# Performance work log

Hardware: AMD Instinct MI355X
Metric: run time of the kernel (lower is better)

Reference implementation:

```python
import jax, jax.numpy as jnp
import numpy as np

STRIDE = 16
A = 9
PRE_NMS_TOP_N = 6000
POST_NMS_TOP_N = 300
NMS_THRESH = 0.7
MIN_SIZE = 16
H, W = 128, 192


def _generate_anchors(base_size=16, ratios=(0.5, 1.0, 2.0), scales=(8, 16, 32)):
    base = np.array([0, 0, base_size - 1, base_size - 1], dtype=np.float64)
    w = base[2] - base[0] + 1
    h = base[3] - base[1] + 1
    x_ctr = base[0] + 0.5 * (w - 1)
    y_ctr = base[1] + 0.5 * (h - 1)
    size = w * h
    ratios = np.array(ratios)
    ws = np.round(np.sqrt(size / ratios))
    hs = np.round(ws * ratios)
    ratio_anchors = np.stack([x_ctr - 0.5 * (ws - 1), y_ctr - 0.5 * (hs - 1),
                              x_ctr + 0.5 * (ws - 1), y_ctr + 0.5 * (hs - 1)], axis=1)
    out = []
    scales = np.array(scales)
    for a in ratio_anchors:
        aw = a[2] - a[0] + 1
        ah = a[3] - a[1] + 1
        xc = a[0] + 0.5 * (aw - 1)
        yc = a[1] + 0.5 * (ah - 1)
        ws2 = aw * scales
        hs2 = ah * scales
        out.append(np.stack([xc - 0.5 * (ws2 - 1), yc - 0.5 * (hs2 - 1),
                             xc + 0.5 * (ws2 - 1), yc + 0.5 * (hs2 - 1)], axis=1))
    return np.concatenate(out, axis=0).astype(np.float32)  # [9,4]


def setup_inputs() -> dict:
    key = jax.random.key(0)
    k1, k2 = jax.random.split(key)
    scores = jax.random.uniform(k1, (1, 2 * A, H, W), dtype=jnp.float32)
    bbox_deltas = 0.1 * jax.random.normal(k2, (1, 4 * A, H, W), dtype=jnp.float32)
    im_info = jnp.array([[H * STRIDE, W * STRIDE, 1.0]], dtype=jnp.float32)
    return {"scores": scores, "bbox_deltas": bbox_deltas, "im_info": im_info}


def _proposal_forward(scores, bbox_deltas, im_info):
    anchors_base = jnp.asarray(_generate_anchors())  # [A,4]
    sc = scores[:, A:, :, :]                          # fg scores [1,A,H,W]
    h, w = sc.shape[-2], sc.shape[-1]
    shift_x = (jnp.arange(w) * STRIDE).astype(sc.dtype)
    shift_y = (jnp.arange(h) * STRIDE).astype(sc.dtype)
    sy, sx = jnp.meshgrid(shift_y, shift_x, indexing='ij')
    shifts = jnp.stack([sx.ravel(), sy.ravel(), sx.ravel(), sy.ravel()], axis=1)  # [K,4]
    anchors = (anchors_base[None, :, :] + shifts[:, None, :]).reshape(-1, 4)      # [K*A,4]

    deltas = bbox_deltas.transpose(0, 2, 3, 1).reshape(-1, 4)
    deltas = jnp.concatenate([deltas[:, :2], jnp.clip(deltas[:, 2:], -10.0, 10.0)], axis=1)
    sc = sc.transpose(0, 2, 3, 1).reshape(-1)  # [K*A]

    widths = anchors[:, 2] - anchors[:, 0] + 1.0
    heights = anchors[:, 3] - anchors[:, 1] + 1.0
    ctr_x = anchors[:, 0] + 0.5 * widths
    ctr_y = anchors[:, 1] + 0.5 * heights
    dx, dy, dw, dh = deltas[:, 0], deltas[:, 1], deltas[:, 2], deltas[:, 3]
    pcx = dx * widths + ctr_x
    pcy = dy * heights + ctr_y
    pw = jnp.exp(dw) * widths
    ph = jnp.exp(dh) * heights
    x1 = pcx - 0.5 * pw
    y1 = pcy - 0.5 * ph
    x2 = pcx + 0.5 * pw
    y2 = pcy + 0.5 * ph

    info = im_info[0]
    x1 = jnp.clip(x1, 0.0, info[1] - 1.0)
    x2 = jnp.clip(x2, 0.0, info[1] - 1.0)
    y1 = jnp.clip(y1, 0.0, info[0] - 1.0)
    y2 = jnp.clip(y2, 0.0, info[0] - 1.0)
    proposals = jnp.stack([x1, y1, x2, y2], axis=1)

    # filter_boxes: mask (instead of dropping) boxes smaller than min_size*scale
    min_sz = MIN_SIZE * info[2]
    valid = ((x2 - x1 + 1.0) >= min_sz) & ((y2 - y1 + 1.0) >= min_sz)
    masked = jnp.where(valid, sc, -jnp.inf)

    # sort desc + pre_nms_topN
    top_scores, top_idx = jax.lax.top_k(masked, PRE_NMS_TOP_N)
    boxes = proposals[top_idx]               # [PRE,4], score-descending
    tvalid = top_scores > -jnp.inf

    # pairwise IoU (torchvision convention)
    area = (boxes[:, 2] - boxes[:, 0]) * (boxes[:, 3] - boxes[:, 1])
    lt = jnp.maximum(boxes[:, None, :2], boxes[None, :, :2])
    rb = jnp.minimum(boxes[:, None, 2:], boxes[None, :, 2:])
    wh = jnp.clip(rb - lt, 0.0)
    inter = wh[..., 0] * wh[..., 1]
    iou = inter / (area[:, None] + area[None, :] - inter)  # [PRE,PRE]

    # greedy NMS over score-sorted boxes
    n = PRE_NMS_TOP_N
    def step(keep, x):
        iou_col, v, i = x
        suppressed = jnp.any(keep & (iou_col > NMS_THRESH))
        k = v & jnp.logical_not(suppressed)
        keep = keep.at[i].set(k)
        return keep, k
    keep, _ = jax.lax.scan(step, jnp.zeros((n,), dtype=bool),
                           (iou.T, tvalid, jnp.arange(n)))

    # kept boxes first (stable => score order preserved), take post_nms_topN
    order = jnp.argsort(jnp.logical_not(keep).astype(jnp.int32), stable=True)[:POST_NMS_TOP_N]
    kept = keep[order]
    out_boxes = jnp.where(kept[:, None], boxes[order], 0.0)
    output = jnp.concatenate(
        [jnp.zeros((POST_NMS_TOP_N, 1), out_boxes.dtype), out_boxes], axis=1)
    return output  # [POST,5]: (batch_idx=0, x1,y1,x2,y2); rows beyond kept count are zero


def reference(scores, bbox_deltas, im_info):
    return _proposal_forward(scores, bbox_deltas, im_info)
```

## Files before the change

### kernel.cpp

```cpp
#include <hip/hip_runtime.h>

#define N_ANCH 221184
#define HW     24576
#define Wd     192
#define AA     9
#define TOPN   6000
#define POSTN  300
#define CAND_CAP 8192
#define NWORDS 94
#define NCHUNK 47

typedef unsigned long long u64;

__device__ const float c_aw[9] = {184.f,368.f,736.f,128.f,256.f,512.f, 88.f,176.f,352.f};
__device__ const float c_ah[9] = { 96.f,192.f,384.f,128.f,256.f,512.f,176.f,352.f,704.f};

__device__ __forceinline__ float4 decode_box(int a, int cell,
                                             const float* __restrict__ deltas,
                                             float info0, float info1, float info2,
                                             bool* valid) {
    int h = cell / Wd;
    int w = cell - h * Wd;
    const float* db = deltas + (size_t)(4 * a) * HW + cell;
    float dx = db[0];
    float dy = db[HW];
    float dw = db[2 * HW];
    float dh = db[3 * HW];
    dw = fminf(fmaxf(dw, -10.f), 10.f);
    dh = fminf(fmaxf(dh, -10.f), 10.f);

    float ww = c_aw[a], hh = c_ah[a];
    float cx = 16.f * (float)w + 8.f;
    float cy = 16.f * (float)h + 8.f;

    float pcx = __fadd_rn(__fmul_rn(dx, ww), cx);
    float pcy = __fadd_rn(__fmul_rn(dy, hh), cy);
    float pw  = __fmul_rn(expf(dw), ww);
    float ph  = __fmul_rn(expf(dh), hh);
    float hpw = __fmul_rn(0.5f, pw);
    float hph = __fmul_rn(0.5f, ph);
    float x1 = __fsub_rn(pcx, hpw);
    float x2 = __fadd_rn(pcx, hpw);
    float y1 = __fsub_rn(pcy, hph);
    float y2 = __fadd_rn(pcy, hph);

    float xmax = __fsub_rn(info1, 1.f);
    float ymax = __fsub_rn(info0, 1.f);
    x1 = fminf(fmaxf(x1, 0.f), xmax);
    x2 = fminf(fmaxf(x2, 0.f), xmax);
    y1 = fminf(fmaxf(y1, 0.f), ymax);
    y2 = fminf(fmaxf(y2, 0.f), ymax);

    float msz = __fmul_rn(16.f, info2);
    *valid = (__fadd_rn(__fsub_rn(x2, x1), 1.f) >= msz) &&
             (__fadd_rn(__fsub_rn(y2, y1), 1.f) >= msz);
    return make_float4(x1, y1, x2, y2);
}

#define ZA_F4 4164
#define ZB_F4 48
#define ZC_F4 64
__global__ __launch_bounds__(256) void init_kernel(float4* zA, float4* zB,
                                                   float4* zC) {
    int t = blockIdx.x * 256 + threadIdx.x;
    float4 z = make_float4(0.f, 0.f, 0.f, 0.f);
    if (t < ZA_F4) zA[t] = z;
    else if (t < ZA_F4 + ZB_F4) zB[t - ZA_F4] = z;
    else if (t < ZA_F4 + ZB_F4 + ZC_F4) zC[t - ZA_F4 - ZB_F4] = z;
}

__global__ __launch_bounds__(256) void decode_kernel(const float* __restrict__ scores,
                                                     const float* __restrict__ deltas,
                                                     const float* __restrict__ iminfo,
                                                     unsigned int* __restrict__ keys,
                                                     unsigned int* __restrict__ hist256) {
    __shared__ unsigned int lh[256];
    lh[threadIdx.x] = 0u;
    __syncthreads();
    int t = blockIdx.x * 256 + threadIdx.x;
    int a = t / HW;
    int cell = t - a * HW;
    float score = scores[(AA + a) * HW + cell];
    bool valid;
    (void)decode_box(a, cell, deltas, iminfo[0], iminfo[1], iminfo[2], &valid);
    unsigned int sb = __float_as_uint(score);
    unsigned int key = valid ? ((sb & 0x80000000u) ? ~sb : (sb | 0x80000000u))
                             : 0x007FFFFFu;
    keys[t] = key;
    atomicAdd(&lh[key >> 24], 1u);
    __syncthreads();
    if (lh[threadIdx.x]) atomicAdd(&hist256[threadIdx.x], lh[threadIdx.x]);
}

__device__ __forceinline__ void scanP(const unsigned int* __restrict__ hist256,
                                      unsigned int* sfx, unsigned int* sP,
                                      unsigned int* sRank, int t) {
    sfx[t] = hist256[t];
    __syncthreads();
    for (int d = 1; d < 256; d <<= 1) {
        unsigned int v = (t + d < 256) ? sfx[t + d] : 0u;
        __syncthreads();
        sfx[t] += v;
        __syncthreads();
    }
    unsigned int ge = sfx[t];
    unsigned int gt = (t < 255) ? sfx[t + 1] : 0u;
    if (ge >= TOPN && gt < TOPN) { *sP = (unsigned int)t; *sRank = TOPN - gt; }
    __syncthreads();
}

__global__ __launch_bounds__(256) void hist2_kernel(const unsigned int* __restrict__ keys,
                                                    const unsigned int* __restrict__ hist256,
                                                    unsigned int* __restrict__ h2) {
    __shared__ unsigned int sfx[256];
    __shared__ unsigned int lh[256];
    __shared__ unsigned int sP, sRank;
    int t = threadIdx.x;
    lh[t] = 0u;
    scanP(hist256, sfx, &sP, &sRank, t);
    unsigned int P = sP;
    unsigned int k = keys[blockIdx.x * 256 + t];
    if ((k >> 24) == P) atomicAdd(&lh[(k >> 16) & 0xFFu], 1u);
    __syncthreads();
    if (lh[t]) atomicAdd(&h2[t], lh[t]);
}

__global__ __launch_bounds__(256) void compact_kernel(const unsigned int* __restrict__ keys,
                                                      const unsigned int* __restrict__ hist256,
                                                      const unsigned int* __restrict__ h2,
                                                      unsigned int* __restrict__ state,
                                                      u64* __restrict__ cand) {
    __shared__ unsigned int sfx[256];
    __shared__ unsigned int sP, sRank, sT;
    int t = threadIdx.x;
    scanP(hist256, sfx, &sP, &sRank, t);
    unsigned int P = sP, rank = sRank;
    __syncthreads();
    sfx[t] = h2[t];
    __syncthreads();
    for (int d = 1; d < 256; d <<= 1) {
        unsigned int v = (t + d < 256) ? sfx[t + d] : 0u;
        __syncthreads();
        sfx[t] += v;
        __syncthreads();
    }
    {
        unsigned int ge = sfx[t];
        unsigned int gt = (t < 255) ? sfx[t + 1] : 0u;
        if (ge >= rank && gt < rank) sT = (P << 24) | ((unsigned int)t << 16);
    }
    __syncthreads();
    unsigned int T = sT;
    int i = blockIdx.x * 256 + t;
    unsigned int k = keys[i];
    if (k >= T) {
        unsigned int pos = atomicAdd(&state[2], 1u);
        if (pos < CAND_CAP) {
            int a = i / HW;
            int cell = i - a * HW;
            unsigned int aidx = (unsigned int)(cell * 9 + a);
            cand[pos] = ((u64)k << 32) | (u64)(~aidx);
        }
    }
}

__global__ __launch_bounds__(256) void rank_scatter_kernel(const u64* __restrict__ cand,
                                                           const float* __restrict__ deltas,
                                                           const float* __restrict__ iminfo,
                                                           float4* __restrict__ tb,
                                                           u64* __restrict__ vmask) {
    __shared__ u64 s[CAND_CAP];
    for (int j = threadIdx.x; j < CAND_CAP; j += 256) s[j] = cand[j];
    int part = threadIdx.x & 7;
    int i = blockIdx.x * 32 + (threadIdx.x >> 3);
    u64 k = cand[i];
    __syncthreads();
    const ulonglong2* sv = (const ulonglong2*)s;
    unsigned int cnt = 0;
    #pragma unroll 8
    for (int jj = part; jj < CAND_CAP / 2; jj += 8) {
        ulonglong2 v = sv[jj];
        cnt += (v.x > k) ? 1u : 0u;
        cnt += (v.y > k) ? 1u : 0u;
    }
    cnt += __shfl_xor(cnt, 1);
    cnt += __shfl_xor(cnt, 2);
    cnt += __shfl_xor(cnt, 4);
    if (part == 0 && k != 0ull && cnt < TOPN) {
        unsigned int aidx = ~((unsigned int)k);
        int a = (int)(aidx % 9u);
        int cell = (int)(aidx / 9u);
        bool valid;
        float4 box = decode_box(a, cell, deltas, iminfo[0], iminfo[1], iminfo[2], &valid);
        tb[cnt] = box;
        if ((unsigned int)(k >> 32) != 0x007FFFFFu)
            atomicOr(&vmask[cnt >> 6], 1ull << (cnt & 63));
    }
}

__global__ __launch_bounds__(64) void nms_matrix_kernel(const float4* __restrict__ tb,
                                                        u64* __restrict__ mat) {
    if (blockIdx.x < blockIdx.y) return;
    __shared__ float4 cb[64];
    int t = threadIdx.x;
    int c0 = blockIdx.x * 64;
    int col = c0 + t;
    cb[t] = (col < TOPN) ? tb[col] : make_float4(0.f, 0.f, 0.f, 0.f);
    __syncthreads();
    int row = blockIdx.y * 64 + t;
    if (row >= TOPN) return;
    float4 rb = tb[row];
    float rA = (rb.z - rb.x) * (rb.w - rb.y);
    u64 mask = 0ull;
    for (int c = 0; c < 64; ++c) {
        if (c0 + c >= TOPN) break;
        float4 b = cb[c];
        float lx = fmaxf(rb.x, b.x), ly = fmaxf(rb.y, b.y);
        float rx = fminf(rb.z, b.z), ry = fminf(rb.w, b.w);
        float iw = fmaxf(rx - lx, 0.f), ih = fmaxf(ry - ly, 0.f);
        float inter = iw * ih;
        float bA = (b.z - b.x) * (b.w - b.y);
        float iou = inter / ((rA + bA) - inter);
        if (iou > 0.7f) mask |= (1ull << c);
    }
    mat[(size_t)row * NWORDS + blockIdx.x] = mask;
}

__device__ __forceinline__ u64 rdl64(u64 v, int l) {
    unsigned int lo = (unsigned int)__builtin_amdgcn_readlane((int)(unsigned int)v, l);
    unsigned int hi = (unsigned int)__builtin_amdgcn_readlane((int)(unsigned int)(v >> 32), l);
    return ((u64)hi << 32) | (u64)lo;
}

__global__ __launch_bounds__(64) void nms_scan_kernel(const u64* __restrict__ mat,
                                                      const u64* __restrict__ vmask,
                                                      const float4* __restrict__ tb,
                                                      float* __restrict__ out) {
    int lane = threadIdx.x;
    u64 r0 = ~vmask[lane];
    u64 r1 = (lane < NWORDS - 64) ? ~vmask[64 + lane] : ~0ull;
    __shared__ int kept[POSTN];
    int cnt = 0;

    u64 a0, a1, b0, b1;
    {
        ulonglong2 vA = *(const ulonglong2*)(mat + (size_t)lane * NWORDS);
        ulonglong2 vB = *(const ulonglong2*)(mat + (size_t)(64 + lane) * NWORDS);
        a0 = vA.x; a1 = vA.y; b0 = vB.x; b1 = vB.y;
    }
    for (int c = 0; c < NCHUNK; ++c) {
        u64 na0 = 0, na1 = 0, nb0 = 0, nb1 = 0;
        if (c + 1 < NCHUNK) {
            const u64* pA = mat + (size_t)((c + 1) * 128 + lane) * NWORDS + 2 * (c + 1);
            const u64* pB = mat + (size_t)((c + 1) * 128 + 64 + lane) * NWORDS + 2 * (c + 1);
            ulonglong2 vA = *(const ulonglong2*)pA;
            ulonglong2 vB = *(const ulonglong2*)pB;
            na0 = vA.x; na1 = vA.y; nb0 = vB.x; nb1 = vB.y;
        }
        int w2 = 2 * c;
        u64 s0 = (w2 < 64) ? rdl64(r0, w2) : rdl64(r1, w2 - 64);
        u64 s1 = (w2 + 1 < 64) ? rdl64(r0, w2 + 1) : rdl64(r1, w2 + 1 - 64);
        if ((s0 & s1) != ~0ull) {
            int base = c * 128;
            u64 rem0 = s0, rem1 = s1, k0 = 0ull, k1 = 0ull;
            while (cnt < POSTN) {
                int b;
                if (~rem0) b = __ffsll((u64)~rem0) - 1;
                else if (~rem1) b = 64 + __ffsll((u64)~rem1) - 1;
                else break;
                if (lane == 0) kept[cnt] = base + b;
                ++cnt;
                u64 w0, w1;
                if (b < 64) {
                    w0 = rdl64(a0, b); w1 = rdl64(a1, b);
                    k0 |= 1ull << b; rem0 |= 1ull << b;
                } else {
                    int bb = b - 64;
                    w0 = rdl64(b0, bb); w1 = rdl64(b1, bb);
                    k1 |= 1ull << bb; rem1 |= 1ull << bb;
                }
                rem0 |= w0; rem1 |= w1;
            }
            if (cnt >= POSTN) break;
            u64 f0 = 0ull, f1 = 0ull, m0 = k0, m1 = k1;
            while (m0 | m1) {
                int idxs[8];
                #pragma unroll
                for (int j = 0; j < 8; ++j) {
                    int b = -1;
                    if (m0) { b = __ffsll(m0) - 1; m0 &= m0 - 1; }
                    else if (m1) { b = 64 + __ffsll(m1) - 1; m1 &= m1 - 1; }
                    idxs[j] = b;
                }
                u64 v0[8], v1[8];
                #pragma unroll
                for (int j = 0; j < 8; ++j) {
                    v0[j] = 0ull; v1[j] = 0ull;
                    if (idxs[j] >= 0) {
                        const u64* row = mat + (size_t)(base + idxs[j]) * NWORDS;
                        v0[j] = row[lane];
                        if (lane < NWORDS - 64) v1[j] = row[64 + lane];
                    }
                }
                #pragma unroll
                for (int j = 0; j < 8; ++j) { f0 |= v0[j]; f1 |= v1[j]; }
            }
            r0 |= f0; r1 |= f1;
        }
        a0 = na0; a1 = na1; b0 = nb0; b1 = nb1;
    }

    for (int r = lane; r < POSTN; r += 64) {
        float4 b = make_float4(0.f, 0.f, 0.f, 0.f);
        if (r < cnt) b = tb[kept[r]];
        float* o = out + r * 5;
        o[0] = 0.f; o[1] = b.x; o[2] = b.y; o[3] = b.z; o[4] = b.w;
    }
}

extern "C" void kernel_launch(void* const* d_in, const int* in_sizes, int n_in,
                              void* d_out, int out_size, void* d_ws, size_t ws_size,
                              hipStream_t stream) {
    const float* scores = (const float*)d_in[0];
    const float* deltas = (const float*)d_in[1];
    const float* iminfo = (const float*)d_in[2];
    float* out = (float*)d_out;

    char* ws = (char*)d_ws;
    unsigned int* keys    = (unsigned int*)(ws + 0);
    unsigned int* hist256 = (unsigned int*)(ws + 884736);
    unsigned int* state   = (unsigned int*)(ws + 885760);
    u64*          cand    = (u64*)(ws + 885824);
    float4*       tb      = (float4*)(ws + 951360);
    u64*          vmask   = (u64*)(ws + 1047616);
    u64*          mat     = (u64*)(ws + 1048384);
    unsigned int* h2      = (unsigned int*)(ws + 1048384);

    const int NB = N_ANCH / 256;

    init_kernel<<<17, 256, 0, stream>>>((float4*)hist256, (float4*)vmask,
                                        (float4*)h2);
    decode_kernel<<<NB, 256, 0, stream>>>(scores, deltas, iminfo, keys, hist256);
    hist2_kernel<<<NB, 256, 0, stream>>>(keys, hist256, h2);
    compact_kernel<<<NB, 256, 0, stream>>>(keys, hist256, h2, state, cand);
    rank_scatter_kernel<<<CAND_CAP / 32, 256, 0, stream>>>(cand, deltas, iminfo, tb, vmask);
    nms_matrix_kernel<<<dim3(NWORDS, NWORDS), 64, 0, stream>>>(tb, mat);
    nms_scan_kernel<<<1, 64, 0, stream>>>(mat, vmask, tb, out);
}
```

Baseline: 241.1 us.

## Fuse init, decode, histogram and compaction into one cooperative grid-synced kernel

Replaces four separate kernels (zero-init, decode and key build, second-level histogram, candidate compaction) with a single cooperative kernel. Stages are separated by grid.sync, and each thread keeps its score key in a register, so the 221K-entry keys array is no longer written to and re-read from global memory. This removes three kernel launches and that memory round trip. In exchange it adds three grid-wide barriers and depends on all 864 blocks being co-resident, which the launch_bounds occupancy hint is meant to allow.

New measurement: 501.8 us. +108.1%, slower.

```diff
diff --git a/kernel.cpp b/kernel.cpp
--- a/kernel.cpp
+++ b/kernel.cpp
@@ -1,4 +1,5 @@
 #include <hip/hip_runtime.h>
+#include <hip/hip_cooperative_groups.h>
 
 #define N_ANCH 221184
 #define HW     24576
@@ -11,6 +12,8 @@
 #define NCHUNK 47
 
 typedef unsigned long long u64;
+
+namespace cg = cooperative_groups;
 
 __device__ const float c_aw[9] = {184.f,368.f,736.f,128.f,256.f,512.f, 88.f,176.f,352.f};
 __device__ const float c_ah[9] = { 96.f,192.f,384.f,128.f,256.f,512.f,176.f,352.f,704.f};
@@ -57,45 +60,48 @@
     return make_float4(x1, y1, x2, y2);
 }
 
-#define ZA_F4 4164
-#define ZB_F4 48
-#define ZC_F4 64
-__global__ __launch_bounds__(256) void init_kernel(float4* zA, float4* zB,
-                                                   float4* zC) {
-    int t = blockIdx.x * 256 + threadIdx.x;
-    float4 z = make_float4(0.f, 0.f, 0.f, 0.f);
-    if (t < ZA_F4) zA[t] = z;
-    else if (t < ZA_F4 + ZB_F4) zB[t - ZA_F4] = z;
-    else if (t < ZA_F4 + ZB_F4 + ZC_F4) zC[t - ZA_F4 - ZB_F4] = z;
-}
-
-__global__ __launch_bounds__(256) void decode_kernel(const float* __restrict__ scores,
-                                                     const float* __restrict__ deltas,
-                                                     const float* __restrict__ iminfo,
-                                                     unsigned int* __restrict__ keys,
-                                                     unsigned int* __restrict__ hist256) {
+#define ZA_U8 8328
+#define ZB_U8 96
+#define ZC_U8 128
+
+__global__ __launch_bounds__(256, 4) void select_kernel(
+        const float* __restrict__ scores,
+        const float* __restrict__ deltas,
+        const float* __restrict__ iminfo,
+        unsigned int* __restrict__ hist256,
+        unsigned int* __restrict__ h2,
+        unsigned int* __restrict__ state,
+        u64* __restrict__ cand,
+        u64* zA, u64* zB, u64* zC) {
+    cg::grid_group grid = cg::this_grid();
     __shared__ unsigned int lh[256];
-    lh[threadIdx.x] = 0u;
-    __syncthreads();
-    int t = blockIdx.x * 256 + threadIdx.x;
-    int a = t / HW;
-    int cell = t - a * HW;
+    __shared__ unsigned int sfx[256];
+    __shared__ unsigned int sP, sRank, sT;
+    const int t = threadIdx.x;
+    const int i = blockIdx.x * 256 + t;
+
+    if (i < ZA_U8) ((volatile u64*)zA)[i] = 0ull;
+    else if (i < ZA_U8 + ZB_U8) ((volatile u64*)zB)[i - ZA_U8] = 0ull;
+    else if (i < ZA_U8 + ZB_U8 + ZC_U8) ((volatile u64*)zC)[i - ZA_U8 - ZB_U8] = 0ull;
+
+    int a = i / HW;
+    int cell = i - a * HW;
     float score = scores[(AA + a) * HW + cell];
     bool valid;
     (void)decode_box(a, cell, deltas, iminfo[0], iminfo[1], iminfo[2], &valid);
     unsigned int sb = __float_as_uint(score);
     unsigned int key = valid ? ((sb & 0x80000000u) ? ~sb : (sb | 0x80000000u))
                              : 0x007FFFFFu;
-    keys[t] = key;
+    grid.sync();
+
+    lh[t] = 0u;
+    __syncthreads();
     atomicAdd(&lh[key >> 24], 1u);
     __syncthreads();
-    if (lh[threadIdx.x]) atomicAdd(&hist256[threadIdx.x], lh[threadIdx.x]);
-}
-
-__device__ __forceinline__ void scanP(const unsigned int* __restrict__ hist256,
-                                      unsigned int* sfx, unsigned int* sP,
-                                      unsigned int* sRank, int t) {
-    sfx[t] = hist256[t];
+    if (lh[t]) atomicAdd(&hist256[t], lh[t]);
+    grid.sync();
+
+    sfx[t] = ((volatile unsigned int*)hist256)[t];
     __syncthreads();
     for (int d = 1; d < 256; d <<= 1) {
         unsigned int v = (t + d < 256) ? sfx[t + d] : 0u;
@@ -103,40 +109,21 @@
         sfx[t] += v;
         __syncthreads();
     }
-    unsigned int ge = sfx[t];
-    unsigned int gt = (t < 255) ? sfx[t + 1] : 0u;
-    if (ge >= TOPN && gt < TOPN) { *sP = (unsigned int)t; *sRank = TOPN - gt; }
-    __syncthreads();
-}
-
-__global__ __launch_bounds__(256) void hist2_kernel(const unsigned int* __restrict__ keys,
-                                                    const unsigned int* __restrict__ hist256,
-                                                    unsigned int* __restrict__ h2) {
-    __shared__ unsigned int sfx[256];
-    __shared__ unsigned int lh[256];
-    __shared__ unsigned int sP, sRank;
-    int t = threadIdx.x;
+    {
+        unsigned int ge = sfx[t];
+        unsigned int gt = (t < 255) ? sfx[t + 1] : 0u;
+        if (ge >= TOPN && gt < TOPN) { sP = (unsigned int)t; sRank = TOPN - gt; }
+    }
+    __syncthreads();
+    unsigned int P = sP, rank = sRank;
     lh[t] = 0u;
-    scanP(hist256, sfx, &sP, &sRank, t);
-    unsigned int P = sP;
-    unsigned int k = keys[blockIdx.x * 256 + t];
-    if ((k >> 24) == P) atomicAdd(&lh[(k >> 16) & 0xFFu], 1u);
+    __syncthreads();
+    if ((key >> 24) == P) atomicAdd(&lh[(key >> 16) & 0xFFu], 1u);
     __syncthreads();
     if (lh[t]) atomicAdd(&h2[t], lh[t]);
-}
-
-__global__ __launch_bounds__(256) void compact_kernel(const unsigned int* __restrict__ keys,
-                                                      const unsigned int* __restrict__ hist256,
-                                                      const unsigned int* __restrict__ h2,
-                                                      unsigned int* __restrict__ state,
-                                                      u64* __restrict__ cand) {
-    __shared__ unsigned int sfx[256];
-    __shared__ unsigned int sP, sRank, sT;
-    int t = threadIdx.x;
-    scanP(hist256, sfx, &sP, &sRank, t);
-    unsigned int P = sP, rank = sRank;
-    __syncthreads();
-    sfx[t] = h2[t];
+    grid.sync();
+
+    sfx[t] = ((volatile unsigned int*)h2)[t];
     __syncthreads();
     for (int d = 1; d < 256; d <<= 1) {
         unsigned int v = (t + d < 256) ? sfx[t + d] : 0u;
@@ -151,15 +138,11 @@
     }
     __syncthreads();
     unsigned int T = sT;
-    int i = blockIdx.x * 256 + t;
-    unsigned int k = keys[i];
-    if (k >= T) {
+    if (key >= T) {
         unsigned int pos = atomicAdd(&state[2], 1u);
         if (pos < CAND_CAP) {
-            int a = i / HW;
-            int cell = i - a * HW;
             unsigned int aidx = (unsigned int)(cell * 9 + a);
-            cand[pos] = ((u64)k << 32) | (u64)(~aidx);
+            cand[pos] = ((u64)key << 32) | (u64)(~aidx);
         }
     }
 }
@@ -327,7 +310,6 @@
     float* out = (float*)d_out;
 
     char* ws = (char*)d_ws;
-    unsigned int* keys    = (unsigned int*)(ws + 0);
     unsigned int* hist256 = (unsigned int*)(ws + 884736);
     unsigned int* state   = (unsigned int*)(ws + 885760);
     u64*          cand    = (u64*)(ws + 885824);
@@ -336,13 +318,19 @@
     u64*          mat     = (u64*)(ws + 1048384);
     unsigned int* h2      = (unsigned int*)(ws + 1048384);
 
+    u64* zA = (u64*)hist256;
+    u64* zB = (u64*)vmask;
+    u64* zC = (u64*)h2;
+
     const int NB = N_ANCH / 256;
 
-    init_kernel<<<17, 256, 0, stream>>>((float4*)hist256, (float4*)vmask,
-                                        (float4*)h2);
-    decode_kernel<<<NB, 256, 0, stream>>>(scores, deltas, iminfo, keys, hist256);
-    hist2_kernel<<<NB, 256, 0, stream>>>(keys, hist256, h2);
-    compact_kernel<<<NB, 256, 0, stream>>>(keys, hist256, h2, state, cand);
+    void* args[] = {
+        (void*)&scores, (void*)&deltas, (void*)&iminfo,
+        (void*)&hist256, (void*)&h2, (void*)&state, (void*)&cand,
+        (void*)&zA, (void*)&zB, (void*)&zC
+    };
+    hipLaunchCooperativeKernel(reinterpret_cast<void*>(select_kernel),
+                               dim3(NB), dim3(256), args, 0, stream);
     rank_scatter_kernel<<<CAND_CAP / 32, 256, 0, stream>>>(cand, deltas, iminfo, tb, vmask);
     nms_matrix_kernel<<<dim3(NWORDS, NWORDS), 64, 0, stream>>>(tb, mat);
     nms_scan_kernel<<<1, 64, 0, stream>>>(mat, vmask, tb, out);
```
